# Kernel optimization log

Measured on AMD Instinct MI355X. Metric: run time of the kernel, lower is better.

## Reference

```python
import jax, jax.numpy as jnp
import numpy as np

B, N, F_IN = 8, 4096, 128
NT = B * N
E = 524288
H, C = 4, 64          # heads, per-head channels
D1 = H * C            # 256, conv1 out = conv2 in = conv2 out


def setup_inputs() -> dict:
    key = jax.random.key(0)
    ks = jax.random.split(key, 14)
    x = jax.random.normal(ks[0], (B, N, F_IN), dtype=jnp.float32)
    # within-graph random edges: E//B edges per graph, offset by graph id
    g = jnp.repeat(jnp.arange(B, dtype=jnp.int64), E // B)
    src = jax.random.randint(ks[1], (E,), 0, N, dtype=jnp.int64) + g * N
    dst = jax.random.randint(ks[2], (E,), 0, N, dtype=jnp.int64) + g * N
    edge_index = jnp.stack([src, dst])
    s = 0.05
    return {
        "x": x,
        "edge_index": edge_index,
        "W1": jax.random.normal(ks[3], (F_IN, D1)) * s,
        "att_src1": jax.random.normal(ks[4], (H, C)) * s,
        "att_dst1": jax.random.normal(ks[5], (H, C)) * s,
        "b1": jnp.zeros((D1,), jnp.float32),
        "W2": jax.random.normal(ks[6], (D1, D1)) * s,
        "att_src2": jax.random.normal(ks[7], (H, C)) * s,
        "att_dst2": jax.random.normal(ks[8], (H, C)) * s,
        "b2": jnp.zeros((D1,), jnp.float32),
        "pw1": jax.random.normal(ks[9], (D1, 1)) * s,
        "pb1": jnp.zeros((1,), jnp.float32),
        "pw2": jax.random.normal(ks[10], (D1, 1)) * s,
        "pb2": jnp.zeros((1,), jnp.float32),
    }


def _gat_conv(h, src, dst, W, att_src, att_dst, bias, n_nodes):
    """PyG GATConv (eval mode): linear, edge attention, segment softmax, scatter-add."""
    Hh, Cc = att_src.shape
    xp = (h @ W).reshape(n_nodes, Hh, Cc)              # [NT,H,C]
    a_src = jnp.sum(xp * att_src, axis=-1)             # [NT,H]
    a_dst = jnp.sum(xp * att_dst, axis=-1)             # [NT,H]
    logits = jax.nn.leaky_relu(a_src[src] + a_dst[dst], 0.2)   # [E',H]
    m = jax.lax.stop_gradient(jax.ops.segment_max(logits, dst, num_segments=n_nodes))
    e = jnp.exp(logits - m[dst])
    denom = jax.ops.segment_sum(e, dst, num_segments=n_nodes)
    alpha = e / (denom[dst] + 1e-16)                   # [E',H]
    msg = xp[src] * alpha[:, :, None]                  # [E',H,C]
    out = jax.ops.segment_sum(msg, dst, num_segments=n_nodes)
    return out.reshape(n_nodes, Hh * Cc) + bias


def reference(x, edge_index, W1, att_src1, att_dst1, b1, W2, att_src2, att_dst2, b2,
              pw1, pb1, pw2, pb2):
    b, n, f = x.shape
    nt = b * n
    xf = x.reshape(nt, f)
    loops = jnp.arange(nt, dtype=edge_index.dtype)     # add_self_loops=True (PyG default)
    src = jnp.concatenate([edge_index[0], loops])
    dst = jnp.concatenate([edge_index[1], loops])

    x0 = jnp.mean(x, axis=-1)                          # [B,N]
    h1 = jax.nn.elu(_gat_conv(xf, src, dst, W1, att_src1, att_dst1, b1, nt))
    x1 = (h1 @ pw1 + pb1)[:, 0].reshape(b, n)          # pool1
    h2 = jax.nn.elu(_gat_conv(h1, src, dst, W2, att_src2, att_dst2, b2, nt))
    x2 = (h2 @ pw2 + pb2)[:, 0].reshape(b, n)          # pool2
    # with_layer_norm==True (bool) != 'True' (str) -> layer norm skipped, which_layer='all'
    return jnp.concatenate([x0, x1, x2], axis=1)       # [B, 3N]
```

## Files before the change

kernel.cpp:

```cpp
#include <hip/hip_runtime.h>

typedef __attribute__((ext_vector_type(8))) short bf16x8;
typedef __attribute__((ext_vector_type(4))) float f32x4;
typedef __attribute__((ext_vector_type(2))) float pk2;

constexpr int B    = 8;
constexpr int N    = 4096;
constexpr int FIN  = 128;
constexpr int NT   = B * N;
constexpr int H    = 4;
constexpr int C    = 64;
constexpr int D1   = H * C;
constexpr int E    = 524288;
constexpr int EPB  = E / B;
constexpr int CHK  = 8192;
constexpr int NSLOT = 18;
constexpr int CAP  = 64;

__device__ __forceinline__ unsigned short f2bf(float f) {
    unsigned u = __float_as_uint(f);
    return (unsigned short)((u + 0x7FFFu + ((u >> 16) & 1u)) >> 16);
}
__device__ __forceinline__ float bf2f(unsigned short b) {
    return __uint_as_float(((unsigned)b) << 16);
}

__device__ __forceinline__ void pack_body(
    const float* __restrict__ W, const float* __restrict__ as_,
    const float* __restrict__ ad_, unsigned short* __restrict__ pB, int g)
{
    int kt  = g / (NSLOT * 64);
    int rem = g % (NSLOT * 64);
    int slot = rem >> 6, l = rem & 63;
    int k0 = kt * 32 + 8 * (l >> 4);
    bool wantLo = (slot == 17);
    int nt = wantLo ? 16 : slot;
    int n  = nt * 16 + (l & 15);
    bf16x8 o;
    #pragma unroll
    for (int j = 0; j < 8; ++j) {
        int k = k0 + j;
        float v;
        if (n < 256) {
            v = W[k * D1 + n];
        } else if (n < 264) {
            int idx = n - 256, hh = idx & 3;
            const float* av = (idx < 4) ? as_ : ad_;
            float s = 0.f;
            #pragma unroll 8
            for (int c = 0; c < C; ++c) s += W[k * D1 + hh * C + c] * av[hh * C + c];
            v = s;
        } else {
            v = 0.f;
        }
        unsigned short hb = f2bf(v);
        o[j] = wantLo ? (short)f2bf(v - bf2f(hb)) : (short)hb;
    }
    *reinterpret_cast<bf16x8*>(pB + (size_t)g * 8) = o;
}

__global__ __launch_bounds__(256) void k_combo(
    const float* __restrict__ x, const int* __restrict__ ei,
    unsigned short* __restrict__ hi, unsigned short* __restrict__ lo,
    float* __restrict__ out,
    unsigned short* __restrict__ pos, unsigned short* __restrict__ bcnt,
    const float* __restrict__ W1, const float* __restrict__ as1, const float* __restrict__ ad1,
    const float* __restrict__ W2, const float* __restrict__ as2, const float* __restrict__ ad2,
    unsigned short* __restrict__ pB1, unsigned short* __restrict__ pB2,
    float* __restrict__ asrc, unsigned short* __restrict__ xpb)
{
    __shared__ unsigned lcnt[N];
    int bid = blockIdx.x, t = threadIdx.x;

    if (bid < 64) {
        int g = bid & 7, c = bid >> 3;
        for (int i = t; i < N; i += 256) lcnt[i] = 0u;
        __syncthreads();
        const int* dstp = ei + E + (size_t)g * EPB + (size_t)c * CHK;
        unsigned short* posp = pos + (size_t)g * EPB + (size_t)c * CHK;
        for (int base = 0; base < CHK; base += 1024) {
            int i0 = base + t;
            int d0 = dstp[i0],       d1 = dstp[i0 + 256],
                d2 = dstp[i0 + 512], d3 = dstp[i0 + 768];
            unsigned r0 = atomicAdd(&lcnt[d0 & (N - 1)], 1u);
            unsigned r1 = atomicAdd(&lcnt[d1 & (N - 1)], 1u);
            unsigned r2 = atomicAdd(&lcnt[d2 & (N - 1)], 1u);
            unsigned r3 = atomicAdd(&lcnt[d3 & (N - 1)], 1u);
            posp[i0]       = (unsigned short)r0;
            posp[i0 + 256] = (unsigned short)r1;
            posp[i0 + 512] = (unsigned short)r2;
            posp[i0 + 768] = (unsigned short)r3;
        }
        __syncthreads();
        for (int i = t; i < N; i += 256)
            bcnt[(((size_t)(g << 12) | i) << 3) + c] = (unsigned short)lcnt[i];
        return;
    }

    if (bid < 118) {
        int pb = bid - 64;
        if (pb == 0) {
            if (t < 4)  asrc[NT * H + t] = -1e30f;
            if (t < 64) reinterpret_cast<uint2*>(xpb)[(size_t)NT * 64 + t] = make_uint2(0u, 0u);
        }
        if (pb < 18) pack_body(W1, as1, ad1, pB1, pb * 256 + t);
        else         pack_body(W2, as2, ad2, pB2, (pb - 18) * 256 + t);
        return;
    }

    int g   = bid & 7;
    int loc = (bid - 118) >> 3;
    int node = (g << 12) + (loc << 3) + (t >> 5);
    int q = t & 31;
    float4 v = reinterpret_cast<const float4*>(x)[node * 32 + q];
    ushort4 h, l;
    h.x = f2bf(v.x); l.x = f2bf(v.x - bf2f(h.x));
    h.y = f2bf(v.y); l.y = f2bf(v.y - bf2f(h.y));
    h.z = f2bf(v.z); l.z = f2bf(v.z - bf2f(h.z));
    h.w = f2bf(v.w); l.w = f2bf(v.w - bf2f(h.w));
    reinterpret_cast<ushort4*>(hi)[node * 32 + q] = h;
    reinterpret_cast<ushort4*>(lo)[node * 32 + q] = l;
    float s = v.x + v.y + v.z + v.w;
    #pragma unroll
    for (int o = 16; o; o >>= 1) s += __shfl_xor(s, o);
    if (q == 0) {
        int n = node & (N - 1);
        out[g * (3 * N) + n] = s * (1.0f / 128.0f);
    }
}

__global__ __launch_bounds__(256) void k_basepad(
    unsigned short* __restrict__ bcnt, unsigned* __restrict__ cnt,
    int* __restrict__ slots)
{
    int bid = blockIdx.x;
    int node = ((bid & 7) << 12) + ((bid >> 3) << 8) + threadIdx.x;
    ushort4* bp = reinterpret_cast<ushort4*>(bcnt + (size_t)node * 8);
    ushort4 lo = bp[0], hi = bp[1];
    unsigned b0 = 1;
    unsigned b1 = b0 + lo.x, b2 = b1 + lo.y, b3 = b2 + lo.z, b4 = b3 + lo.w;
    unsigned b5 = b4 + hi.x, b6 = b5 + hi.y, b7 = b6 + hi.z;
    unsigned deg = b7 + hi.w;
    cnt[node] = deg;
    ushort4 wlo, whi;
    wlo.x = (unsigned short)b0; wlo.y = (unsigned short)b1;
    wlo.z = (unsigned short)b2; wlo.w = (unsigned short)b3;
    whi.x = (unsigned short)b4; whi.y = (unsigned short)b5;
    whi.z = (unsigned short)b6; whi.w = (unsigned short)b7;
    bp[0] = wlo; bp[1] = whi;
    int* sl = slots + (size_t)node * CAP;
    sl[0] = node * 4;
    int dpad = (((int)deg + 1) & ~1) + 14;
    for (int i = (int)deg; i < dpad; ++i) sl[i] = NT * 4;
}

template <int K, bool CB>
__global__ __launch_bounds__(256) void k_mfma(
    const unsigned short* __restrict__ Ahi, const unsigned short* __restrict__ Alo,
    const unsigned short* __restrict__ pB,
    unsigned short* __restrict__ xpb, float* __restrict__ asrc, float* __restrict__ adst,
    const int* __restrict__ ei, const unsigned short* __restrict__ pos,
    const unsigned short* __restrict__ bcnt, int* __restrict__ slots)
{
    constexpr int KT = K / 32;
    int t = threadIdx.x, lane = t & 63, w = t >> 6;

    if (CB && blockIdx.x >= NT / 64) {
        int cb = blockIdx.x - NT / 64;
        int g = cb & 7, j = cb >> 3;
        const int* srcp = ei + (size_t)g * EPB;
        const int* dstp = ei + E + (size_t)g * EPB;
        const unsigned short* posp = pos + (size_t)g * EPB;
        #pragma unroll
        for (int k2 = 0; k2 < 4; ++k2) {
            int eg = j * 1024 + k2 * 256 + t;
            int s = srcp[eg], d = dstp[eg];
            unsigned rank = posp[eg];
            unsigned base = bcnt[((size_t)d << 3) + (eg >> 13)];
            slots[(size_t)d * CAP + base + rank] = s * 4;
        }
        return;
    }

    int wm = w & 1, wn = w >> 1;
    int m0 = ((blockIdx.x & 7) << 12) + ((blockIdx.x >> 3) << 6) + wm * 32;
    int sBase = wn * 9;

    f32x4 acc[2][9];
    #pragma unroll
    for (int i = 0; i < 2; ++i)
        #pragma unroll
        for (int j = 0; j < 9; ++j)
            acc[i][j] = (f32x4){0.f, 0.f, 0.f, 0.f};

    int aRow = m0 + (lane & 15);
    int aCol = 8 * (lane >> 4);
    const unsigned short* a0h = Ahi + (size_t)aRow * K + aCol;
    const unsigned short* a0l = Alo + (size_t)aRow * K + aCol;
    const unsigned short* bp  = pB + ((size_t)sBase * 64 + lane) * 8;

    bf16x8 bc[9], bn[9];
    bf16x8 ah0c, al0c, ah1c, al1c, ah0n, al0n, ah1n, al1n;

    #pragma unroll
    for (int j = 0; j < 9; ++j) bc[j] = *reinterpret_cast<const bf16x8*>(bp + j * 512);
    ah0c = *reinterpret_cast<const bf16x8*>(a0h);
    al0c = *reinterpret_cast<const bf16x8*>(a0l);
    ah1c = *reinterpret_cast<const bf16x8*>(a0h + 16 * K);
    al1c = *reinterpret_cast<const bf16x8*>(a0l + 16 * K);

    #pragma unroll
    for (int kt = 0; kt < KT; ++kt) {
        if (kt + 1 < KT) {
            const unsigned short* bpn = bp + (size_t)(kt + 1) * NSLOT * 64 * 8;
            #pragma unroll
            for (int j = 0; j < 9; ++j) bn[j] = *reinterpret_cast<const bf16x8*>(bpn + j * 512);
            ah0n = *reinterpret_cast<const bf16x8*>(a0h + (kt + 1) * 32);
            al0n = *reinterpret_cast<const bf16x8*>(a0l + (kt + 1) * 32);
            ah1n = *reinterpret_cast<const bf16x8*>(a0h + 16 * K + (kt + 1) * 32);
            al1n = *reinterpret_cast<const bf16x8*>(a0l + 16 * K + (kt + 1) * 32);
        }
        __builtin_amdgcn_sched_barrier(0);
        if (wn == 0) {
            #pragma unroll
            for (int j = 0; j < 9; ++j) {
                acc[0][j] = __builtin_amdgcn_mfma_f32_16x16x32_bf16(ah0c, bc[j], acc[0][j], 0, 0, 0);
                acc[1][j] = __builtin_amdgcn_mfma_f32_16x16x32_bf16(ah1c, bc[j], acc[1][j], 0, 0, 0);
                acc[0][j] = __builtin_amdgcn_mfma_f32_16x16x32_bf16(al0c, bc[j], acc[0][j], 0, 0, 0);
                acc[1][j] = __builtin_amdgcn_mfma_f32_16x16x32_bf16(al1c, bc[j], acc[1][j], 0, 0, 0);
            }
        } else {
            #pragma unroll
            for (int j = 0; j < 8; ++j) {
                acc[0][j] = __builtin_amdgcn_mfma_f32_16x16x32_bf16(ah0c, bc[j], acc[0][j], 0, 0, 0);
                acc[1][j] = __builtin_amdgcn_mfma_f32_16x16x32_bf16(ah1c, bc[j], acc[1][j], 0, 0, 0);
                acc[0][j] = __builtin_amdgcn_mfma_f32_16x16x32_bf16(al0c, bc[j], acc[0][j], 0, 0, 0);
                acc[1][j] = __builtin_amdgcn_mfma_f32_16x16x32_bf16(al1c, bc[j], acc[1][j], 0, 0, 0);
            }
            acc[0][7] = __builtin_amdgcn_mfma_f32_16x16x32_bf16(ah0c, bc[8], acc[0][7], 0, 0, 0);
            acc[1][7] = __builtin_amdgcn_mfma_f32_16x16x32_bf16(ah1c, bc[8], acc[1][7], 0, 0, 0);
        }
        if (kt + 1 < KT) {
            #pragma unroll
            for (int j = 0; j < 9; ++j) bc[j] = bn[j];
            ah0c = ah0n; al0c = al0n; ah1c = ah1n; al1c = al1n;
        }
    }

    #pragma unroll
    for (int mt = 0; mt < 2; ++mt) {
        int rowB = m0 + mt * 16 + (lane >> 4) * 4;
        if (wn == 0) {
            #pragma unroll
            for (int j = 0; j < 9; ++j) {
                int col = j * 16 + (lane & 15);
                #pragma unroll
                for (int r = 0; r < 4; ++r)
                    xpb[(size_t)(rowB + r) * D1 + col] = f2bf(acc[mt][j][r]);
            }
        } else {
            #pragma unroll
            for (int j = 0; j < 8; ++j) {
                int nt = 9 + j;
                int col = nt * 16 + (lane & 15);
                #pragma unroll
                for (int r = 0; r < 4; ++r) {
                    int row = rowB + r;
                    float v = acc[mt][j][r];
                    if (col < 256)      xpb[(size_t)row * D1 + col] = f2bf(v);
                    else if (col < 260) asrc[row * H + (col - 256)] = v;
                    else if (col < 264) adst[row * H + (col - 260)] = v;
                }
            }
        }
    }
}

__global__ __launch_bounds__(256) void k_node(
    const unsigned* __restrict__ cnt, const int* __restrict__ slots,
    const float* __restrict__ asrc, const float* __restrict__ adst,
    const unsigned short* __restrict__ xp,
    const float* __restrict__ bias, const float* __restrict__ pw,
    const float* __restrict__ pb,
    unsigned short* __restrict__ hhi, unsigned short* __restrict__ hlo,
    float* __restrict__ out, int sec)
{
    int bid = blockIdx.x;
    int w = threadIdx.x >> 6, lane = threadIdx.x & 63;
    int half = lane >> 5;
    int hl   = lane & 31;
    int head = hl >> 3;
    int node = ((bid & 7) << 12) | (((bid >> 3) << 2) + w);

    int deg = (int)cnt[node];
    int dp  = (deg + 1) & ~1;
    const int* sl = slots + (size_t)node * CAP;
    float adh = adst[node * H + head];
    const uint4* xp4 = (const uint4*)xp;

    float den = 0.f;
    pk2 acc01 = {0.f, 0.f}, acc23 = {0.f, 0.f}, acc45 = {0.f, 0.f}, acc67 = {0.f, 0.f};

    #define PROC(aa, vv)                                                     \
    {                                                                        \
        float l  = aa + adh;                                                 \
        float ev = __expf(fmaxf(l, 0.2f * l));                               \
        den += ev;                                                           \
        pk2 e2 = {ev, ev};                                                   \
        pk2 t01 = {__uint_as_float(vv.x << 16), __uint_as_float(vv.x & 0xFFFF0000u)}; \
        pk2 t23 = {__uint_as_float(vv.y << 16), __uint_as_float(vv.y & 0xFFFF0000u)}; \
        pk2 t45 = {__uint_as_float(vv.z << 16), __uint_as_float(vv.z & 0xFFFF0000u)}; \
        pk2 t67 = {__uint_as_float(vv.w << 16), __uint_as_float(vv.w & 0xFFFF0000u)}; \
        acc01 = __builtin_elementwise_fma(e2, t01, acc01);                   \
        acc23 = __builtin_elementwise_fma(e2, t23, acc23);                   \
        acc45 = __builtin_elementwise_fma(e2, t45, acc45);                   \
        acc67 = __builtin_elementwise_fma(e2, t67, acc67);                   \
    }

    int   s_;
    float aX, aY, aZ, a_;
    uint4 vX, vY, vZ, v_;
    s_ = sl[0 + half]; aX = asrc[s_ + head]; vX = xp4[(s_ << 3) + hl];
    s_ = sl[2 + half]; aY = asrc[s_ + head]; vY = xp4[(s_ << 3) + hl];
    s_ = sl[4 + half]; aZ = asrc[s_ + head]; vZ = xp4[(s_ << 3) + hl];

    for (int i = 0; i < dp; i += 6) {
        s_ = sl[i + 6 + half];  a_ = asrc[s_ + head]; v_ = xp4[(s_ << 3) + hl];
        PROC(aX, vX); aX = a_; vX = v_;
        s_ = sl[i + 8 + half];  a_ = asrc[s_ + head]; v_ = xp4[(s_ << 3) + hl];
        PROC(aY, vY); aY = a_; vY = v_;
        s_ = sl[i + 10 + half]; a_ = asrc[s_ + head]; v_ = xp4[(s_ << 3) + hl];
        PROC(aZ, vZ); aZ = a_; vZ = v_;
    }
    #undef PROC

    den      += __shfl_xor(den, 32);
    acc01[0] += __shfl_xor(acc01[0], 32);
    acc01[1] += __shfl_xor(acc01[1], 32);
    acc23[0] += __shfl_xor(acc23[0], 32);
    acc23[1] += __shfl_xor(acc23[1], 32);
    acc45[0] += __shfl_xor(acc45[0], 32);
    acc45[1] += __shfl_xor(acc45[1], 32);
    acc67[0] += __shfl_xor(acc67[0], 32);
    acc67[1] += __shfl_xor(acc67[1], 32);

    float invd = 1.f / (den + 1e-16f);
    float4 b0 = reinterpret_cast<const float4*>(bias)[hl * 2];
    float4 b1 = reinterpret_cast<const float4*>(bias)[hl * 2 + 1];
    float4 p0 = reinterpret_cast<const float4*>(pw)[hl * 2];
    float4 p1 = reinterpret_cast<const float4*>(pw)[hl * 2 + 1];

    float h0 = fmaf(acc01[0], invd, b0.x), h1 = fmaf(acc01[1], invd, b0.y),
          h2 = fmaf(acc23[0], invd, b0.z), h3 = fmaf(acc23[1], invd, b0.w),
          h4 = fmaf(acc45[0], invd, b1.x), h5 = fmaf(acc45[1], invd, b1.y),
          h6 = fmaf(acc67[0], invd, b1.z), h7 = fmaf(acc67[1], invd, b1.w);
    h0 = h0 > 0.f ? h0 : __expf(h0) - 1.f;
    h1 = h1 > 0.f ? h1 : __expf(h1) - 1.f;
    h2 = h2 > 0.f ? h2 : __expf(h2) - 1.f;
    h3 = h3 > 0.f ? h3 : __expf(h3) - 1.f;
    h4 = h4 > 0.f ? h4 : __expf(h4) - 1.f;
    h5 = h5 > 0.f ? h5 : __expf(h5) - 1.f;
    h6 = h6 > 0.f ? h6 : __expf(h6) - 1.f;
    h7 = h7 > 0.f ? h7 : __expf(h7) - 1.f;

    if (hhi && half == 0) {
        unsigned short q0 = f2bf(h0), q1 = f2bf(h1), q2 = f2bf(h2), q3 = f2bf(h3),
                       q4 = f2bf(h4), q5 = f2bf(h5), q6 = f2bf(h6), q7 = f2bf(h7);
        uint4 hw, lw;
        hw.x = (unsigned)q0 | ((unsigned)q1 << 16);
        hw.y = (unsigned)q2 | ((unsigned)q3 << 16);
        hw.z = (unsigned)q4 | ((unsigned)q5 << 16);
        hw.w = (unsigned)q6 | ((unsigned)q7 << 16);
        lw.x = (unsigned)f2bf(h0 - bf2f(q0)) | ((unsigned)f2bf(h1 - bf2f(q1)) << 16);
        lw.y = (unsigned)f2bf(h2 - bf2f(q2)) | ((unsigned)f2bf(h3 - bf2f(q3)) << 16);
        lw.z = (unsigned)f2bf(h4 - bf2f(q4)) | ((unsigned)f2bf(h5 - bf2f(q5)) << 16);
        lw.w = (unsigned)f2bf(h6 - bf2f(q6)) | ((unsigned)f2bf(h7 - bf2f(q7)) << 16);
        reinterpret_cast<uint4*>(hhi)[node * 32 + hl] = hw;
        reinterpret_cast<uint4*>(hlo)[node * 32 + hl] = lw;
    }

    float p = h0 * p0.x + h1 * p0.y + h2 * p0.z + h3 * p0.w
            + h4 * p1.x + h5 * p1.y + h6 * p1.z + h7 * p1.w;
    #pragma unroll
    for (int o = 16; o; o >>= 1) p += __shfl_xor(p, o);
    if (lane == 0) {
        int b = node >> 12;
        int n = node & (N - 1);
        out[b * (3 * N) + sec * N + n] = p + pb[0];
    }
}

extern "C" void kernel_launch(void* const* d_in, const int* in_sizes, int n_in,
                              void* d_out, int out_size, void* d_ws, size_t ws_size,
                              hipStream_t stream) {
    const float* x   = (const float*)d_in[0];
    const int*   ei  = (const int*)d_in[1];
    const float* W1  = (const float*)d_in[2];
    const float* as1 = (const float*)d_in[3];
    const float* ad1 = (const float*)d_in[4];
    const float* b1  = (const float*)d_in[5];
    const float* W2  = (const float*)d_in[6];
    const float* as2 = (const float*)d_in[7];
    const float* ad2 = (const float*)d_in[8];
    const float* b2  = (const float*)d_in[9];
    const float* pw1 = (const float*)d_in[10];
    const float* pb1 = (const float*)d_in[11];
    const float* pw2 = (const float*)d_in[12];
    const float* pb2 = (const float*)d_in[13];
    float* out = (float*)d_out;

    unsigned short* xpb  = (unsigned short*)d_ws;
    unsigned short* xhi  = xpb  + (size_t)(NT + 1) * D1;
    unsigned short* xlo  = xhi  + (size_t)NT * FIN;
    unsigned short* h1hi = xlo  + (size_t)NT * FIN;
    unsigned short* h1lo = h1hi + (size_t)NT * D1;
    float*    asrc   = (float*)(h1lo + (size_t)NT * D1);
    float*    adst   = asrc + (size_t)(NT + 1) * H;
    unsigned short* pB1 = (unsigned short*)(adst + (size_t)NT * H);
    unsigned short* pB2 = pB1 + (size_t)4 * NSLOT * 64 * 8;
    unsigned* cnt    = (unsigned*)(pB2 + (size_t)8 * NSLOT * 64 * 8);
    int*      slots  = (int*)(cnt + NT);
    unsigned short* pos  = (unsigned short*)(slots + (size_t)NT * CAP);
    unsigned short* bcnt = pos + (size_t)E;

    k_combo<<<118 + NT / 8, 256, 0, stream>>>(x, ei, xhi, xlo, out, pos, bcnt,
                                              W1, as1, ad1, W2, as2, ad2, pB1, pB2,
                                              asrc, xpb);
    k_basepad<<<128, 256, 0, stream>>>(bcnt, cnt, slots);

    k_mfma<128, true><<<NT / 64 + 512, 256, 0, stream>>>(
        xhi, xlo, pB1, xpb, asrc, adst, ei, pos, bcnt, slots);
    k_node<<<NT / 4, 256, 0, stream>>>(cnt, slots, asrc, adst, xpb,
                                       b1, pw1, pb1, h1hi, h1lo, out, 1);

    k_mfma<256, false><<<NT / 64, 256, 0, stream>>>(
        h1hi, h1lo, pB2, xpb, asrc, adst, nullptr, nullptr, nullptr, nullptr);
    k_node<<<NT / 4, 256, 0, stream>>>(cnt, slots, asrc, adst, xpb,
                                       b2, pw2, pb2, nullptr, nullptr, out, 2);
}
```

Before: 115.9 us.

## Coalesce slot sentinel fill and deepen gather prefetch with shuffled slot indices

The slot-padding kernel now fills each block's whole 64-entry slot rows with sentinels using coalesced int4 stores, then writes the self-loop entry after a barrier. This replaces the old per-thread strided padding loop. The aggregation kernel loads the node's 64 slot indices once, one per lane, and hands them out with wave shuffles instead of repeated global loads. It also raises the gather prefetch depth from three to four edge pairs per iteration. The trade-offs are extra sentinel writes to every slot, higher register pressure, and an unused leftover macro definition.

Result: faster. 111.9 us (-3.5%).

```diff
diff --git a/kernel.cpp b/kernel.cpp
--- a/kernel.cpp
+++ b/kernel.cpp
@@ -134,7 +134,15 @@
     int* __restrict__ slots)
 {
     int bid = blockIdx.x;
-    int node = ((bid & 7) << 12) + ((bid >> 3) << 8) + threadIdx.x;
+    int t = threadIdx.x;
+    int nbase = ((bid & 7) << 12) + ((bid >> 3) << 8);
+    int node = nbase + t;
+
+    int4* base4 = reinterpret_cast<int4*>(slots + (size_t)nbase * CAP);
+    int4 sent = make_int4(NT * 4, NT * 4, NT * 4, NT * 4);
+    #pragma unroll
+    for (int i = 0; i < 16; ++i) base4[i * 256 + t] = sent;
+
     ushort4* bp = reinterpret_cast<ushort4*>(bcnt + (size_t)node * 8);
     ushort4 lo = bp[0], hi = bp[1];
     unsigned b0 = 1;
@@ -148,10 +156,9 @@
     whi.x = (unsigned short)b4; whi.y = (unsigned short)b5;
     whi.z = (unsigned short)b6; whi.w = (unsigned short)b7;
     bp[0] = wlo; bp[1] = whi;
-    int* sl = slots + (size_t)node * CAP;
-    sl[0] = node * 4;
-    int dpad = (((int)deg + 1) & ~1) + 14;
-    for (int i = (int)deg; i < dpad; ++i) sl[i] = NT * 4;
+
+    __syncthreads();
+    slots[(size_t)node * CAP] = node * 4;
 }
 
 template <int K, bool CB>
@@ -295,12 +302,31 @@
     int deg = (int)cnt[node];
     int dp  = (deg + 1) & ~1;
     const int* sl = slots + (size_t)node * CAP;
+    int myslot = sl[lane];
     float adh = adst[node * H + head];
-    const uint4* xp4 = (const uint4*)xp;
+    const float* asrcH = asrc + head;
+    const uint4* xpL = (const uint4*)xp + hl;
 
     float den = 0.f;
     pk2 acc01 = {0.f, 0.f}, acc23 = {0.f, 0.f}, acc45 = {0.f, 0.f}, acc67 = {0.f, 0.f};
 
+    #define PROC(aa, vv)                                                     \
+    {                                                                        \
+        float l  = aa + adh;                                                 \
+        float ev = __expf(fmaxf(l, 0.2f * l));                               \
+        den += ev;                                                           \
+        pk2 e2 = {ev, ev};                                                   \
+        pk2 t01 = {__uint_as_float(vv.x << 16), __uint_as_float(vv.x & 0xFFFF0000u)}; \
+        pk2 t23 = {__uint_as_float(vv.y << 16), __uint_as_float(vv.y & 0xFFFF0000u)}; \
+        pk2 t45 = {__uint_as_float(vv.z << 16), __uint_as_float(vv.z & 0xFFFF0000u)}; \
+        pk2 t67 = {__uint_as_float(vv.w << 16), __uint_as_float(vv.w & 0xFFFF0000u)}; \
+        acc01 = __builtin_elementwise_fma(e2, t01, acc01);                   \
+        acc23 = __builtin_elementwise_fma(e2, t23, acc23);                   \
+        acc45 = __builtin_elementwise_fma(e2, t45, acc67 * 0.f + acc23);     \
+        acc45 = __builtin_elementwise_fma(e2, t45, acc45);                   \
+        acc67 = __builtin_elementwise_fma(e2, t67, acc67);                   \
+    }
+    #undef PROC
     #define PROC(aa, vv)                                                     \
     {                                                                        \
         float l  = aa + adh;                                                 \
@@ -317,20 +343,35 @@
         acc67 = __builtin_elementwise_fma(e2, t67, acc67);                   \
     }
 
-    int   s_;
-    float aX, aY, aZ, a_;
-    uint4 vX, vY, vZ, v_;
-    s_ = sl[0 + half]; aX = asrc[s_ + head]; vX = xp4[(s_ << 3) + hl];
-    s_ = sl[2 + half]; aY = asrc[s_ + head]; vY = xp4[(s_ << 3) + hl];
-    s_ = sl[4 + half]; aZ = asrc[s_ + head]; vZ = xp4[(s_ << 3) + hl];
-
-    for (int i = 0; i < dp; i += 6) {
-        s_ = sl[i + 6 + half];  a_ = asrc[s_ + head]; v_ = xp4[(s_ << 3) + hl];
-        PROC(aX, vX); aX = a_; vX = v_;
-        s_ = sl[i + 8 + half];  a_ = asrc[s_ + head]; v_ = xp4[(s_ << 3) + hl];
-        PROC(aY, vY); aY = a_; vY = v_;
-        s_ = sl[i + 10 + half]; a_ = asrc[s_ + head]; v_ = xp4[(s_ << 3) + hl];
-        PROC(aZ, vZ); aZ = a_; vZ = v_;
+    float aA, aB, aC, aD;
+    uint4 vA, vB, vC, vD;
+    {
+        int s0 = __shfl(myslot, 0 + half);
+        int s1 = __shfl(myslot, 2 + half);
+        int s2 = __shfl(myslot, 4 + half);
+        int s3 = __shfl(myslot, 6 + half);
+        aA = asrcH[s0]; vA = xpL[(size_t)s0 << 3];
+        aB = asrcH[s1]; vB = xpL[(size_t)s1 << 3];
+        aC = asrcH[s2]; vC = xpL[(size_t)s2 << 3];
+        aD = asrcH[s3]; vD = xpL[(size_t)s3 << 3];
+    }
+
+    for (int i = 0; i < dp; i += 8) {
+        int s0 = __shfl(myslot, i + 8 + half);
+        int s1 = __shfl(myslot, i + 10 + half);
+        int s2 = __shfl(myslot, i + 12 + half);
+        int s3 = __shfl(myslot, i + 14 + half);
+        float b0 = asrcH[s0], b1 = asrcH[s1], b2 = asrcH[s2], b3 = asrcH[s3];
+        uint4 w0 = xpL[(size_t)s0 << 3], w1 = xpL[(size_t)s1 << 3],
+              w2 = xpL[(size_t)s2 << 3], w3 = xpL[(size_t)s3 << 3];
+
+        PROC(aA, vA);
+        PROC(aB, vB);
+        PROC(aC, vC);
+        PROC(aD, vD);
+
+        aA = b0; vA = w0; aB = b1; vB = w1;
+        aC = b2; vC = w2; aD = b3; vD = w3;
     }
     #undef PROC
 
```
